# Kernel tuning notes

Measured on AMD Instinct MI355X. Metric: run time of the kernel, lower is better.

The kernel has to match this reference:

```python
import jax, jax.numpy as jnp
import numpy as np

N, E = 50000, 800000
IN, H, OUT = 128, 128, 64
N_MID = 4  # middle GIN layers (num_layers=6 -> 1 first + 4 mid + 1 last)


def setup_inputs() -> dict:
    key = jax.random.key(0)
    ks = jax.random.split(key, 8)
    def w(k, shape, fan_in):
        return (jax.random.normal(k, shape, jnp.float32) / np.sqrt(fan_in)).astype(jnp.float32)
    x = jax.random.normal(ks[0], (N, IN), jnp.float32)
    edge_index = jax.random.randint(ks[1], (2, E), 0, N, dtype=jnp.int64)
    return {
        "x": x,
        "edge_index": edge_index,
        "w0a": w(ks[2], (IN, H), IN), "b0a": jnp.zeros((H,), jnp.float32),
        "w0b": w(ks[3], (H, H), H),   "b0b": jnp.zeros((H,), jnp.float32),
        "wma": w(ks[4], (N_MID, H, H), H), "bma": jnp.zeros((N_MID, H), jnp.float32),
        "wmb": w(ks[5], (N_MID, H, H), H), "bmb": jnp.zeros((N_MID, H), jnp.float32),
        "wl": w(ks[6], (H, OUT), H), "bl": jnp.zeros((OUT,), jnp.float32),
    }


def reference(x, edge_index, w0a, b0a, w0b, b0b, wma, bma, wmb, bmb, wl, bl):
    n = x.shape[0]
    src, dst = edge_index[0], edge_index[1]

    def gin_agg(h):
        # GIN with eps=0: (1+eps)*h_i + sum_{j->i} h_j
        return h + jax.ops.segment_sum(h[src], dst, num_segments=n)

    # layer 0: Lin(IN,H)-ReLU-Lin(H,H), then inter-layer ReLU
    h = gin_agg(x)
    h = jax.nn.relu(jax.nn.relu(h @ w0a + b0a) @ w0b + b0b)

    # middle layers 1..4 (scan over stacked params)
    def body(h, p):
        wa, ba, wb, bb = p
        g = gin_agg(h)
        g = jax.nn.relu(g @ wa + ba) @ wb + bb
        return jax.nn.relu(g), None

    h, _ = jax.lax.scan(body, h, (wma, bma, wmb, bmb))

    # last layer: single Lin(H,OUT), then sigmoid
    h = gin_agg(h) @ wl + bl
    return jax.nn.sigmoid(h)
```

## Files before the change

kernel.cpp:

```cpp
#include <hip/hip_runtime.h>
#include <hip/hip_bf16.h>

#define HDIM 128

typedef __attribute__((ext_vector_type(8))) short bf16x8;
typedef __attribute__((ext_vector_type(4))) float f32x4;

__device__ __forceinline__ unsigned short bf16_rne(float x) {
    unsigned int u = __float_as_uint(x);
    unsigned int r = u + 0x7FFFu + ((u >> 16) & 1u);
    return (unsigned short)(r >> 16);
}


__global__ __launch_bounds__(256) void hist_kernel(const int* __restrict__ ei, int E,
                                                   int* __restrict__ deg) {
    int e = blockIdx.x * 256 + threadIdx.x;
    if (e < E) atomicAdd(&deg[ei[E + e]], 1);
}

__global__ __launch_bounds__(256) void scan1_kernel(const int* __restrict__ deg,
                                                    int* __restrict__ rowp,
                                                    int* __restrict__ bsum, int N) {
    __shared__ int s[256];
    int t = threadIdx.x;
    int i = blockIdx.x * 256 + t;
    int v = (i < N) ? deg[i] : 0;
    s[t] = v; __syncthreads();
    for (int off = 1; off < 256; off <<= 1) {
        int x = (t >= off) ? s[t - off] : 0;
        __syncthreads();
        s[t] += x;
        __syncthreads();
    }
    if (i < N) rowp[i] = s[t] - v;
    if (t == 255) bsum[blockIdx.x] = s[255];
}

__global__ __launch_bounds__(256) void scan2_kernel(int* __restrict__ bsum, int NB) {
    __shared__ int s[256];
    int t = threadIdx.x;
    int v = (t < NB) ? bsum[t] : 0;
    s[t] = v; __syncthreads();
    for (int off = 1; off < 256; off <<= 1) {
        int x = (t >= off) ? s[t - off] : 0;
        __syncthreads();
        s[t] += x;
        __syncthreads();
    }
    if (t < NB) bsum[t] = s[t] - v;
}

__global__ __launch_bounds__(256) void scan3_kernel(int* __restrict__ rowp,
                                                    const int* __restrict__ bsum,
                                                    int* __restrict__ cur, int N, int E) {
    int i = blockIdx.x * 256 + threadIdx.x;
    if (i < N) {
        int r = rowp[i] + bsum[blockIdx.x];
        rowp[i] = r;
        cur[i] = r;
    }
    if (i == 0) rowp[N] = E;
}

template <typename IT>
__global__ __launch_bounds__(256) void scatter_kernel(const int* __restrict__ ei, int E,
                                                      int* __restrict__ cur,
                                                      IT* __restrict__ srcs) {
    int e = blockIdx.x * 256 + threadIdx.x;
    if (e < E) {
        int d = ei[E + e];
        int p = atomicAdd(&cur[d], 1);
        srcs[p] = (IT)ei[e];
    }
}


__global__ __launch_bounds__(256) void pack_w_kernel(const float* __restrict__ w0a,
                                                     const float* __restrict__ w0b,
                                                     const float* __restrict__ wma,
                                                     const float* __restrict__ wmb,
                                                     short* __restrict__ wpack) {
    int idx = blockIdx.x * 256 + threadIdx.x;
    if (idx >= 10 * 16384) return;
    int mat = idx >> 14;
    int rem = idx & 16383;
    int i = rem & 7;
    int lane = (rem >> 3) & 63;
    int kc = (rem >> 9) & 3;
    int ct = rem >> 11;
    const float* W = (mat == 0) ? w0a
                   : (mat == 1) ? w0b
                   : (mat < 6)  ? (wma + (size_t)(mat - 2) * 16384)
                                : (wmb + (size_t)(mat - 6) * 16384);
    int k = kc * 32 + (lane >> 4) * 8 + i;
    int col = ct * 16 + (lane & 15);
    float x = W[k * 128 + col];
    unsigned short hb = bf16_rne(x);
    float hf = __uint_as_float(((unsigned int)hb) << 16);
    unsigned short lb = bf16_rne(x - hf);
    wpack[(size_t)mat * 32768 + rem] = (short)hb;
    wpack[(size_t)mat * 32768 + 16384 + rem] = (short)lb;
}


template <typename IT>
__global__ __launch_bounds__(256) void agg_slice_kernel(const float* __restrict__ h,
                                                        const int* __restrict__ rowp,
                                                        const IT* __restrict__ srcs,
                                                        float* __restrict__ out, int N) {
    const int tid = threadIdx.x;
    const int g = blockIdx.x & 7;
    const int chunk = blockIdx.x >> 3;
    const int grp = tid >> 2;
    const int l = tid & 3;
    const int node = chunk * 64 + grp;
    if (node >= N) return;

    const float4* h4 = (const float4*)h;
    const int cbase = g * 4 + l;

    int beg = rowp[node], end = rowp[node + 1];
    int em1 = max(end - 1, 0);

    const float4 z = {0.f, 0.f, 0.f, 0.f};
    float4 a0 = h4[(size_t)node * 32 + cbase];
    float4 a1 = z, a2 = z, a3 = z, a4 = z, a5 = z, a6 = z, a7 = z;

    for (int q = beg; q < end; q += 8) {
        int c0 = min(q + 0, em1);
        int c1 = min(q + 1, em1);
        int c2 = min(q + 2, em1);
        int c3 = min(q + 3, em1);
        int c4 = min(q + 4, em1);
        int c5 = min(q + 5, em1);
        int c6 = min(q + 6, em1);
        int c7 = min(q + 7, em1);
        int s0 = (int)srcs[c0];
        int s1 = (int)srcs[c1];
        int s2 = (int)srcs[c2];
        int s3 = (int)srcs[c3];
        int s4 = (int)srcs[c4];
        int s5 = (int)srcs[c5];
        int s6 = (int)srcs[c6];
        int s7 = (int)srcs[c7];
        float4 v0 = h4[(size_t)s0 * 32 + cbase];
        float4 v1 = h4[(size_t)s1 * 32 + cbase];
        float4 v2 = h4[(size_t)s2 * 32 + cbase];
        float4 v3 = h4[(size_t)s3 * 32 + cbase];
        float4 v4 = h4[(size_t)s4 * 32 + cbase];
        float4 v5 = h4[(size_t)s5 * 32 + cbase];
        float4 v6 = h4[(size_t)s6 * 32 + cbase];
        float4 v7 = h4[(size_t)s7 * 32 + cbase];
        float m0 = (q + 0 < end) ? 1.f : 0.f;
        float m1 = (q + 1 < end) ? 1.f : 0.f;
        float m2 = (q + 2 < end) ? 1.f : 0.f;
        float m3 = (q + 3 < end) ? 1.f : 0.f;
        float m4 = (q + 4 < end) ? 1.f : 0.f;
        float m5 = (q + 5 < end) ? 1.f : 0.f;
        float m6 = (q + 6 < end) ? 1.f : 0.f;
        float m7 = (q + 7 < end) ? 1.f : 0.f;
        a0.x = fmaf(v0.x, m0, a0.x); a0.y = fmaf(v0.y, m0, a0.y);
        a0.z = fmaf(v0.z, m0, a0.z); a0.w = fmaf(v0.w, m0, a0.w);
        a1.x = fmaf(v1.x, m1, a1.x); a1.y = fmaf(v1.y, m1, a1.y);
        a1.z = fmaf(v1.z, m1, a1.z); a1.w = fmaf(v1.w, m1, a1.w);
        a2.x = fmaf(v2.x, m2, a2.x); a2.y = fmaf(v2.y, m2, a2.y);
        a2.z = fmaf(v2.z, m2, a2.z); a2.w = fmaf(v2.w, m2, a2.w);
        a3.x = fmaf(v3.x, m3, a3.x); a3.y = fmaf(v3.y, m3, a3.y);
        a3.z = fmaf(v3.z, m3, a3.z); a3.w = fmaf(v3.w, m3, a3.w);
        a4.x = fmaf(v4.x, m4, a4.x); a4.y = fmaf(v4.y, m4, a4.y);
        a4.z = fmaf(v4.z, m4, a4.z); a4.w = fmaf(v4.w, m4, a4.w);
        a5.x = fmaf(v5.x, m5, a5.x); a5.y = fmaf(v5.y, m5, a5.y);
        a5.z = fmaf(v5.z, m5, a5.z); a5.w = fmaf(v5.w, m5, a5.w);
        a6.x = fmaf(v6.x, m6, a6.x); a6.y = fmaf(v6.y, m6, a6.y);
        a6.z = fmaf(v6.z, m6, a6.z); a6.w = fmaf(v6.w, m6, a6.w);
        a7.x = fmaf(v7.x, m7, a7.x); a7.y = fmaf(v7.y, m7, a7.y);
        a7.z = fmaf(v7.z, m7, a7.z); a7.w = fmaf(v7.w, m7, a7.w);
    }

    a0.x = ((a0.x + a1.x) + (a2.x + a3.x)) + ((a4.x + a5.x) + (a6.x + a7.x));
    a0.y = ((a0.y + a1.y) + (a2.y + a3.y)) + ((a4.y + a5.y) + (a6.y + a7.y));
    a0.z = ((a0.z + a1.z) + (a2.z + a3.z)) + ((a4.z + a5.z) + (a6.z + a7.z));
    a0.w = ((a0.w + a1.w) + (a2.w + a3.w)) + ((a4.w + a5.w) + (a6.w + a7.w));
    ((float4*)out)[(size_t)node * 32 + cbase] = a0;
}


template <typename IT>
__global__ __launch_bounds__(256) void agg_out_kernel(const float* __restrict__ t,
                                                      const int* __restrict__ rowp,
                                                      const IT* __restrict__ srcs,
                                                      const float* __restrict__ bias,
                                                      float* __restrict__ out, int N) {
    int lane = threadIdx.x & 63;
    int node = blockIdx.x * 4 + (threadIdx.x >> 6);
    if (node >= N) return;
    int beg = rowp[node], end = rowp[node + 1];
    float a0 = t[node * 64 + lane];
    float a1 = 0.f, a2 = 0.f, a3 = 0.f, a4 = 0.f, a5 = 0.f, a6 = 0.f, a7 = 0.f;
    int p = beg;
    for (; p + 8 <= end; p += 8) {
        int s0 = (int)srcs[p + 0];
        int s1 = (int)srcs[p + 1];
        int s2 = (int)srcs[p + 2];
        int s3 = (int)srcs[p + 3];
        int s4 = (int)srcs[p + 4];
        int s5 = (int)srcs[p + 5];
        int s6 = (int)srcs[p + 6];
        int s7 = (int)srcs[p + 7];
        a0 += t[s0 * 64 + lane];
        a1 += t[s1 * 64 + lane];
        a2 += t[s2 * 64 + lane];
        a3 += t[s3 * 64 + lane];
        a4 += t[s4 * 64 + lane];
        a5 += t[s5 * 64 + lane];
        a6 += t[s6 * 64 + lane];
        a7 += t[s7 * 64 + lane];
    }
    for (; p < end; ++p) a0 += t[(int)srcs[p] * 64 + lane];
    float z = a0 + ((a1 + a2) + (a3 + a4)) + ((a5 + a6) + a7) + bias[lane];
    out[node * 64 + lane] = 1.f / (1.f + __expf(-z));
}


__device__ __forceinline__ void cvt8(const float4 p, const float4 q,
                                     bf16x8& hi, bf16x8& lo) {
    unsigned short hb; float hf;
#define CVT1(IDX, V) \
    hb = bf16_rne(V); hf = __uint_as_float(((unsigned int)hb) << 16); \
    hi[IDX] = (short)hb; lo[IDX] = (short)bf16_rne((V) - hf);
    CVT1(0, p.x) CVT1(1, p.y) CVT1(2, p.z) CVT1(3, p.w)
    CVT1(4, q.x) CVT1(5, q.y) CVT1(6, q.z) CVT1(7, q.w)
#undef CVT1
}

template <bool WRITE_GLOBAL>
__device__ __forceinline__ void gemm_phase_mfma(float* __restrict__ myrows,
                                                const short* __restrict__ wp,
                                                const float* __restrict__ bias,
                                                int arow, int agrp,
                                                int l, float* __restrict__ gout,
                                                int row_base, int N) {
    f32x4 acc[8];
#pragma unroll
    for (int ct = 0; ct < 8; ++ct) acc[ct] = (f32x4){0.f, 0.f, 0.f, 0.f};

    const short* wlo = wp + 16384;
#pragma unroll
    for (int kc = 0; kc < 4; ++kc) {
        const float* ap = &myrows[arow * 132 + kc * 32 + agrp * 8];
        float4 p = *(const float4*)ap;
        float4 q = *(const float4*)(ap + 4);
        bf16x8 ahi, alo;
        cvt8(p, q, ahi, alo);
#pragma unroll
        for (int ct = 0; ct < 8; ++ct) {
            const int off = ((ct * 4 + kc) << 9) + (l << 3);
            bf16x8 bhi = *(const bf16x8*)(wp + off);
            bf16x8 blo = *(const bf16x8*)(wlo + off);
            acc[ct] = __builtin_amdgcn_mfma_f32_16x16x32_bf16(ahi, bhi, acc[ct], 0, 0, 0);
            acc[ct] = __builtin_amdgcn_mfma_f32_16x16x32_bf16(alo, bhi, acc[ct], 0, 0, 0);
            acc[ct] = __builtin_amdgcn_mfma_f32_16x16x32_bf16(ahi, blo, acc[ct], 0, 0, 0);
            acc[ct] = __builtin_amdgcn_mfma_f32_16x16x32_bf16(alo, blo, acc[ct], 0, 0, 0);
        }
    }

#pragma unroll
    for (int ct = 0; ct < 8; ++ct) {
        float bv = bias[ct * 16 + arow];
#pragma unroll
        for (int r = 0; r < 4; ++r) {
            float v = fmaxf(acc[ct][r] + bv, 0.f);
            if (WRITE_GLOBAL) {
                int row = row_base + agrp * 4 + r;
                if (row < N) gout[(size_t)row * 128 + ct * 16 + arow] = v;
            } else {
                myrows[(agrp * 4 + r) * 132 + ct * 16 + arow] = v;
            }
        }
    }
}

__global__ __launch_bounds__(256, 4) void mlp2_mfma_kernel(
    const float* __restrict__ in,
    const short* __restrict__ wpa, const float* __restrict__ ba,
    const short* __restrict__ wpb, const float* __restrict__ bb,
    float* __restrict__ out, int N) {
    __shared__ float sh[64 * 132];
    const int tid = threadIdx.x;
    const int wave = tid >> 6;
    const int l = tid & 63;
    const int arow = l & 15;
    const int agrp = l >> 4;
    const int row0 = blockIdx.x * 64;

    const float4* in4 = (const float4*)in;
#pragma unroll
    for (int it = 0; it < 8; ++it) {
        int i = tid + it * 256;
        int r = i >> 5, c = i & 31;
        int row = row0 + r;
        float4 z = {0.f, 0.f, 0.f, 0.f};
        float4 v = (row < N) ? in4[(size_t)row * 32 + c] : z;
        *(float4*)&sh[r * 132 + c * 4] = v;
    }
    __syncthreads();

    float* myrows = &sh[wave * 16 * 132];
    gemm_phase_mfma<false>(myrows, wpa, ba, arow, agrp, l, nullptr, 0, N);
    __syncthreads();
    gemm_phase_mfma<true>(myrows, wpb, bb, arow, agrp, l, out, row0 + wave * 16, N);
}


__global__ __launch_bounds__(256, 6) void gemm64_kernel(const float* __restrict__ in,
                                                        const float* __restrict__ W,
                                                        float* __restrict__ out, int N) {
    constexpr int TX = 16, RPT = 2;
    __shared__ float4 sh[32 * 32];

    int tid = threadIdx.x;
    int tx = tid % TX;
    int ty = tid / TX;
    int row0 = blockIdx.x * 32;

    const float4* in4 = (const float4*)in;
    for (int i = tid; i < 32 * 32; i += 256) {
        int r = i >> 5, c = i & 31;
        int row = row0 + r;
        float4 z = {0.f, 0.f, 0.f, 0.f};
        sh[i] = (row < N) ? in4[(size_t)row * 32 + c] : z;
    }
    __syncthreads();

    const float4* W4 = (const float4*)W;
    float acc[RPT][4];
#pragma unroll
    for (int r = 0; r < RPT; ++r)
#pragma unroll
        for (int c = 0; c < 4; ++c) acc[r][c] = 0.f;

#pragma unroll 4
    for (int kk = 0; kk < 128; kk += 4) {
        float4 w0 = W4[(kk + 0) * TX + tx];
        float4 w1 = W4[(kk + 1) * TX + tx];
        float4 w2 = W4[(kk + 2) * TX + tx];
        float4 w3 = W4[(kk + 3) * TX + tx];
#pragma unroll
        for (int r = 0; r < RPT; ++r) {
            float4 hv = sh[(ty * RPT + r) * 32 + (kk >> 2)];
            acc[r][0] += hv.x * w0.x + hv.y * w1.x + hv.z * w2.x + hv.w * w3.x;
            acc[r][1] += hv.x * w0.y + hv.y * w1.y + hv.z * w2.y + hv.w * w3.y;
            acc[r][2] += hv.x * w0.z + hv.y * w1.z + hv.z * w2.z + hv.w * w3.z;
            acc[r][3] += hv.x * w0.w + hv.y * w1.w + hv.z * w2.w + hv.w * w3.w;
        }
    }

#pragma unroll
    for (int r = 0; r < RPT; ++r) {
        int row = row0 + ty * RPT + r;
        if (row < N) {
            float4 v = {acc[r][0], acc[r][1], acc[r][2], acc[r][3]};
            ((float4*)out)[(size_t)row * TX + tx] = v;
        }
    }
}


template <typename IT>
static void run_graph(const float* x, const int* ei, int N, int E,
                      const float* w0a, const float* b0a, const float* w0b, const float* b0b,
                      const float* wma, const float* bma, const float* wmb, const float* bmb,
                      const float* wl, const float* bl,
                      float* A, float* B, int* deg, int* rowp, int* cur, int* bsum,
                      IT* srcs, short* wpack, float* out, hipStream_t stream) {
    const int NB = (N + 255) / 256;
    dim3 blk(256);

    pack_w_kernel<<<(10 * 16384 + 255) / 256, blk, 0, stream>>>(w0a, w0b, wma, wmb, wpack);

    hipMemsetAsync(deg, 0, (size_t)N * sizeof(int), stream);
    hist_kernel<<<(E + 255) / 256, blk, 0, stream>>>(ei, E, deg);
    scan1_kernel<<<NB, blk, 0, stream>>>(deg, rowp, bsum, N);
    scan2_kernel<<<1, blk, 0, stream>>>(bsum, NB);
    scan3_kernel<<<NB, blk, 0, stream>>>(rowp, bsum, cur, N, E);
    scatter_kernel<IT><<<(E + 255) / 256, blk, 0, stream>>>(ei, E, cur, srcs);

    const int slice_grid = 8 * ((N + 63) / 64);
    const int aggo_grid  = (N + 3) / 4;
    const int m64_grid   = (N + 63) / 64;
    const int g32_grid   = (N + 31) / 32;

    agg_slice_kernel<IT><<<slice_grid, blk, 0, stream>>>(x, rowp, srcs, A, N);
    mlp2_mfma_kernel<<<m64_grid, blk, 0, stream>>>(A, wpack + 0, b0a,
                                                   wpack + 32768, b0b, B, N);

    float* h = B;
    float* o = A;
    for (int l = 0; l < 4; ++l) {
        const short* wpa = wpack + (size_t)(2 + l) * 32768;
        const short* wpb = wpack + (size_t)(6 + l) * 32768;
        const float* ba = bma + (size_t)l * HDIM;
        const float* bb = bmb + (size_t)l * HDIM;
        agg_slice_kernel<IT><<<slice_grid, blk, 0, stream>>>(h, rowp, srcs, o, N);
        mlp2_mfma_kernel<<<m64_grid, blk, 0, stream>>>(o, wpa, ba, wpb, bb, h, N);
    }

    gemm64_kernel<<<g32_grid, blk, 0, stream>>>(h, wl, o, N);
    agg_out_kernel<IT><<<aggo_grid, blk, 0, stream>>>(o, rowp, srcs, bl, out, N);
}

extern "C" void kernel_launch(void* const* d_in, const int* in_sizes, int n_in,
                              void* d_out, int out_size, void* d_ws, size_t ws_size,
                              hipStream_t stream) {
    const float* x   = (const float*)d_in[0];
    const int*   ei  = (const int*)d_in[1];
    const float* w0a = (const float*)d_in[2];
    const float* b0a = (const float*)d_in[3];
    const float* w0b = (const float*)d_in[4];
    const float* b0b = (const float*)d_in[5];
    const float* wma = (const float*)d_in[6];
    const float* bma = (const float*)d_in[7];
    const float* wmb = (const float*)d_in[8];
    const float* bmb = (const float*)d_in[9];
    const float* wl  = (const float*)d_in[10];
    const float* bl  = (const float*)d_in[11];

    const int N = in_sizes[0] / HDIM;
    const int E = in_sizes[1] / 2;

    float* A = (float*)d_ws;
    float* B = A + (size_t)N * HDIM;
    int* deg  = (int*)(B + (size_t)N * HDIM);
    int* rowp = deg + N;
    int* cur  = rowp + N + 1;
    int* bsum = cur + N;
    int* srcs = bsum + 256;
    short* wpack = (short*)(srcs + E);

    if (N <= 65535) {
        run_graph<unsigned short>(x, ei, N, E, w0a, b0a, w0b, b0b, wma, bma, wmb, bmb,
                                  wl, bl, A, B, deg, rowp, cur, bsum,
                                  (unsigned short*)srcs, wpack, (float*)d_out, stream);
    } else {
        run_graph<int>(x, ei, N, E, w0a, b0a, w0b, b0b, wma, bma, wmb, bmb,
                       wl, bl, A, B, deg, rowp, cur, bsum,
                       srcs, wpack, (float*)d_out, stream);
    }
}
```

Before: 666.5 us.

## Make aggregation persistent with XCD-affine feature-slice work queues

Replaces the fixed-grid feature-slice aggregation with a persistent kernel of 2048 blocks. Each block reads its hardware XCC id and first drains an atomic work queue for the matching 16-column feature slice, then moves on to the other slices. The aim is to keep each slice's gathered rows in a single XCD's L2 cache and to balance work dynamically. In exchange it adds a global atomic and two block barriers per 64-node chunk, plus per-layer counters that must be zeroed with a memset.

```diff
diff --git a/kernel.cpp b/kernel.cpp
--- a/kernel.cpp
+++ b/kernel.cpp
@@ -105,84 +105,97 @@
 
 
 template <typename IT>
-__global__ __launch_bounds__(256) void agg_slice_kernel(const float* __restrict__ h,
-                                                        const int* __restrict__ rowp,
-                                                        const IT* __restrict__ srcs,
-                                                        float* __restrict__ out, int N) {
+__global__ __launch_bounds__(256) void agg_xcd_kernel(const float* __restrict__ h,
+                                                      const int* __restrict__ rowp,
+                                                      const IT* __restrict__ srcs,
+                                                      float* __restrict__ out, int N,
+                                                      int* __restrict__ cnt) {
+    __shared__ int s_task;
+    const int nchunks = (N + 63) >> 6;
     const int tid = threadIdx.x;
-    const int g = blockIdx.x & 7;
-    const int chunk = blockIdx.x >> 3;
     const int grp = tid >> 2;
     const int l = tid & 3;
-    const int node = chunk * 64 + grp;
-    if (node >= N) return;
+
+    int myx = __builtin_amdgcn_s_getreg(20 | (0 << 6) | (31 << 11)) & 7;
 
     const float4* h4 = (const float4*)h;
-    const int cbase = g * 4 + l;
-
-    int beg = rowp[node], end = rowp[node + 1];
-    int em1 = max(end - 1, 0);
-
-    const float4 z = {0.f, 0.f, 0.f, 0.f};
-    float4 a0 = h4[(size_t)node * 32 + cbase];
-    float4 a1 = z, a2 = z, a3 = z, a4 = z, a5 = z, a6 = z, a7 = z;
-
-    for (int q = beg; q < end; q += 8) {
-        int c0 = min(q + 0, em1);
-        int c1 = min(q + 1, em1);
-        int c2 = min(q + 2, em1);
-        int c3 = min(q + 3, em1);
-        int c4 = min(q + 4, em1);
-        int c5 = min(q + 5, em1);
-        int c6 = min(q + 6, em1);
-        int c7 = min(q + 7, em1);
-        int s0 = (int)srcs[c0];
-        int s1 = (int)srcs[c1];
-        int s2 = (int)srcs[c2];
-        int s3 = (int)srcs[c3];
-        int s4 = (int)srcs[c4];
-        int s5 = (int)srcs[c5];
-        int s6 = (int)srcs[c6];
-        int s7 = (int)srcs[c7];
-        float4 v0 = h4[(size_t)s0 * 32 + cbase];
-        float4 v1 = h4[(size_t)s1 * 32 + cbase];
-        float4 v2 = h4[(size_t)s2 * 32 + cbase];
-        float4 v3 = h4[(size_t)s3 * 32 + cbase];
-        float4 v4 = h4[(size_t)s4 * 32 + cbase];
-        float4 v5 = h4[(size_t)s5 * 32 + cbase];
-        float4 v6 = h4[(size_t)s6 * 32 + cbase];
-        float4 v7 = h4[(size_t)s7 * 32 + cbase];
-        float m0 = (q + 0 < end) ? 1.f : 0.f;
-        float m1 = (q + 1 < end) ? 1.f : 0.f;
-        float m2 = (q + 2 < end) ? 1.f : 0.f;
-        float m3 = (q + 3 < end) ? 1.f : 0.f;
-        float m4 = (q + 4 < end) ? 1.f : 0.f;
-        float m5 = (q + 5 < end) ? 1.f : 0.f;
-        float m6 = (q + 6 < end) ? 1.f : 0.f;
-        float m7 = (q + 7 < end) ? 1.f : 0.f;
-        a0.x = fmaf(v0.x, m0, a0.x); a0.y = fmaf(v0.y, m0, a0.y);
-        a0.z = fmaf(v0.z, m0, a0.z); a0.w = fmaf(v0.w, m0, a0.w);
-        a1.x = fmaf(v1.x, m1, a1.x); a1.y = fmaf(v1.y, m1, a1.y);
-        a1.z = fmaf(v1.z, m1, a1.z); a1.w = fmaf(v1.w, m1, a1.w);
-        a2.x = fmaf(v2.x, m2, a2.x); a2.y = fmaf(v2.y, m2, a2.y);
-        a2.z = fmaf(v2.z, m2, a2.z); a2.w = fmaf(v2.w, m2, a2.w);
-        a3.x = fmaf(v3.x, m3, a3.x); a3.y = fmaf(v3.y, m3, a3.y);
-        a3.z = fmaf(v3.z, m3, a3.z); a3.w = fmaf(v3.w, m3, a3.w);
-        a4.x = fmaf(v4.x, m4, a4.x); a4.y = fmaf(v4.y, m4, a4.y);
-        a4.z = fmaf(v4.z, m4, a4.z); a4.w = fmaf(v4.w, m4, a4.w);
-        a5.x = fmaf(v5.x, m5, a5.x); a5.y = fmaf(v5.y, m5, a5.y);
-        a5.z = fmaf(v5.z, m5, a5.z); a5.w = fmaf(v5.w, m5, a5.w);
-        a6.x = fmaf(v6.x, m6, a6.x); a6.y = fmaf(v6.y, m6, a6.y);
-        a6.z = fmaf(v6.z, m6, a6.z); a6.w = fmaf(v6.w, m6, a6.w);
-        a7.x = fmaf(v7.x, m7, a7.x); a7.y = fmaf(v7.y, m7, a7.y);
-        a7.z = fmaf(v7.z, m7, a7.z); a7.w = fmaf(v7.w, m7, a7.w);
-    }
-
-    a0.x = ((a0.x + a1.x) + (a2.x + a3.x)) + ((a4.x + a5.x) + (a6.x + a7.x));
-    a0.y = ((a0.y + a1.y) + (a2.y + a3.y)) + ((a4.y + a5.y) + (a6.y + a7.y));
-    a0.z = ((a0.z + a1.z) + (a2.z + a3.z)) + ((a4.z + a5.z) + (a6.z + a7.z));
-    a0.w = ((a0.w + a1.w) + (a2.w + a3.w)) + ((a4.w + a5.w) + (a6.w + a7.w));
-    ((float4*)out)[(size_t)node * 32 + cbase] = a0;
+
+    for (int gi = 0; gi < 8; ++gi) {
+        const int g = (myx + gi) & 7;
+        const int cbase = g * 4 + l;
+        for (;;) {
+            if (tid == 0) s_task = atomicAdd(&cnt[g], 1);
+            __syncthreads();
+            const int t = s_task;
+            __syncthreads();
+            if (t >= nchunks) break;
+
+            const int node = t * 64 + grp;
+            if (node < N) {
+                int beg = rowp[node], end = rowp[node + 1];
+                int em1 = max(end - 1, 0);
+                const float4 z = {0.f, 0.f, 0.f, 0.f};
+                float4 a0 = h4[(size_t)node * 32 + cbase];
+                float4 a1 = z, a2 = z, a3 = z, a4 = z, a5 = z, a6 = z, a7 = z;
+
+                for (int q = beg; q < end; q += 8) {
+                    int c0 = min(q + 0, em1);
+                    int c1 = min(q + 1, em1);
+                    int c2 = min(q + 2, em1);
+                    int c3 = min(q + 3, em1);
+                    int c4 = min(q + 4, em1);
+                    int c5 = min(q + 5, em1);
+                    int c6 = min(q + 6, em1);
+                    int c7 = min(q + 7, em1);
+                    int s0 = (int)srcs[c0];
+                    int s1 = (int)srcs[c1];
+                    int s2 = (int)srcs[c2];
+                    int s3 = (int)srcs[c3];
+                    int s4 = (int)srcs[c4];
+                    int s5 = (int)srcs[c5];
+                    int s6 = (int)srcs[c6];
+                    int s7 = (int)srcs[c7];
+                    float4 v0 = h4[(size_t)s0 * 32 + cbase];
+                    float4 v1 = h4[(size_t)s1 * 32 + cbase];
+                    float4 v2 = h4[(size_t)s2 * 32 + cbase];
+                    float4 v3 = h4[(size_t)s3 * 32 + cbase];
+                    float4 v4 = h4[(size_t)s4 * 32 + cbase];
+                    float4 v5 = h4[(size_t)s5 * 32 + cbase];
+                    float4 v6 = h4[(size_t)s6 * 32 + cbase];
+                    float4 v7 = h4[(size_t)s7 * 32 + cbase];
+                    float m0 = (q + 0 < end) ? 1.f : 0.f;
+                    float m1 = (q + 1 < end) ? 1.f : 0.f;
+                    float m2 = (q + 2 < end) ? 1.f : 0.f;
+                    float m3 = (q + 3 < end) ? 1.f : 0.f;
+                    float m4 = (q + 4 < end) ? 1.f : 0.f;
+                    float m5 = (q + 5 < end) ? 1.f : 0.f;
+                    float m6 = (q + 6 < end) ? 1.f : 0.f;
+                    float m7 = (q + 7 < end) ? 1.f : 0.f;
+                    a0.x = fmaf(v0.x, m0, a0.x); a0.y = fmaf(v0.y, m0, a0.y);
+                    a0.z = fmaf(v0.z, m0, a0.z); a0.w = fmaf(v0.w, m0, a0.w);
+                    a1.x = fmaf(v1.x, m1, a1.x); a1.y = fmaf(v1.y, m1, a1.y);
+                    a1.z = fmaf(v1.z, m1, a1.z); a1.w = fmaf(v1.w, m1, a1.w);
+                    a2.x = fmaf(v2.x, m2, a2.x); a2.y = fmaf(v2.y, m2, a2.y);
+                    a2.z = fmaf(v2.z, m2, a2.z); a2.w = fmaf(v2.w, m2, a2.w);
+                    a3.x = fmaf(v3.x, m3, a3.x); a3.y = fmaf(v3.y, m3, a3.y);
+                    a3.z = fmaf(v3.z, m3, a3.z); a3.w = fmaf(v3.w, m3, a3.w);
+                    a4.x = fmaf(v4.x, m4, a4.x); a4.y = fmaf(v4.y, m4, a4.y);
+                    a4.z = fmaf(v4.z, m4, a4.z); a4.w = fmaf(v4.w, m4, a4.w);
+                    a5.x = fmaf(v5.x, m5, a5.x); a5.y = fmaf(v5.y, m5, a5.y);
+                    a5.z = fmaf(v5.z, m5, a5.z); a5.w = fmaf(v5.w, m5, a5.w);
+                    a6.x = fmaf(v6.x, m6, a6.x); a6.y = fmaf(v6.y, m6, a6.y);
+                    a6.z = fmaf(v6.z, m6, a6.z); a6.w = fmaf(v6.w, m6, a6.w);
+                    a7.x = fmaf(v7.x, m7, a7.x); a7.y = fmaf(v7.y, m7, a7.y);
+                    a7.z = fmaf(v7.z, m7, a7.z); a7.w = fmaf(v7.w, m7, a7.w);
+                }
+                a0.x = ((a0.x + a1.x) + (a2.x + a3.x)) + ((a4.x + a5.x) + (a6.x + a7.x));
+                a0.y = ((a0.y + a1.y) + (a2.y + a3.y)) + ((a4.y + a5.y) + (a6.y + a7.y));
+                a0.z = ((a0.z + a1.z) + (a2.z + a3.z)) + ((a4.z + a5.z) + (a6.z + a7.z));
+                a0.w = ((a0.w + a1.w) + (a2.w + a3.w)) + ((a4.w + a5.w) + (a6.w + a7.w));
+                ((float4*)out)[(size_t)node * 32 + cbase] = a0;
+            }
+        }
+    }
 }
 
 
@@ -373,25 +386,26 @@
                       const float* wma, const float* bma, const float* wmb, const float* bmb,
                       const float* wl, const float* bl,
                       float* A, float* B, int* deg, int* rowp, int* cur, int* bsum,
-                      IT* srcs, short* wpack, float* out, hipStream_t stream) {
+                      IT* srcs, short* wpack, int* qcnt, float* out, hipStream_t stream) {
     const int NB = (N + 255) / 256;
     dim3 blk(256);
 
     pack_w_kernel<<<(10 * 16384 + 255) / 256, blk, 0, stream>>>(w0a, w0b, wma, wmb, wpack);
 
     hipMemsetAsync(deg, 0, (size_t)N * sizeof(int), stream);
+    hipMemsetAsync(qcnt, 0, 5 * 8 * sizeof(int), stream);
     hist_kernel<<<(E + 255) / 256, blk, 0, stream>>>(ei, E, deg);
     scan1_kernel<<<NB, blk, 0, stream>>>(deg, rowp, bsum, N);
     scan2_kernel<<<1, blk, 0, stream>>>(bsum, NB);
     scan3_kernel<<<NB, blk, 0, stream>>>(rowp, bsum, cur, N, E);
     scatter_kernel<IT><<<(E + 255) / 256, blk, 0, stream>>>(ei, E, cur, srcs);
 
-    const int slice_grid = 8 * ((N + 63) / 64);
-    const int aggo_grid  = (N + 3) / 4;
-    const int m64_grid   = (N + 63) / 64;
-    const int g32_grid   = (N + 31) / 32;
-
-    agg_slice_kernel<IT><<<slice_grid, blk, 0, stream>>>(x, rowp, srcs, A, N);
+    const int agg_grid  = 2048;
+    const int aggo_grid = (N + 3) / 4;
+    const int m64_grid  = (N + 63) / 64;
+    const int g32_grid  = (N + 31) / 32;
+
+    agg_xcd_kernel<IT><<<agg_grid, blk, 0, stream>>>(x, rowp, srcs, A, N, qcnt + 0);
     mlp2_mfma_kernel<<<m64_grid, blk, 0, stream>>>(A, wpack + 0, b0a,
                                                    wpack + 32768, b0b, B, N);
 
@@ -402,7 +416,8 @@
         const short* wpb = wpack + (size_t)(6 + l) * 32768;
         const float* ba = bma + (size_t)l * HDIM;
         const float* bb = bmb + (size_t)l * HDIM;
-        agg_slice_kernel<IT><<<slice_grid, blk, 0, stream>>>(h, rowp, srcs, o, N);
+        agg_xcd_kernel<IT><<<agg_grid, blk, 0, stream>>>(h, rowp, srcs, o, N,
+                                                         qcnt + 8 * (l + 1));
         mlp2_mfma_kernel<<<m64_grid, blk, 0, stream>>>(o, wpa, ba, wpb, bb, h, N);
     }
 
@@ -437,14 +452,16 @@
     int* bsum = cur + N;
     int* srcs = bsum + 256;
     short* wpack = (short*)(srcs + E);
+    int* qcnt = (int*)(wpack + 10 * 32768);
 
     if (N <= 65535) {
         run_graph<unsigned short>(x, ei, N, E, w0a, b0a, w0b, b0b, wma, bma, wmb, bmb,
                                   wl, bl, A, B, deg, rowp, cur, bsum,
-                                  (unsigned short*)srcs, wpack, (float*)d_out, stream);
+                                  (unsigned short*)srcs, wpack, qcnt,
+                                  (float*)d_out, stream);
     } else {
         run_graph<int>(x, ei, N, E, w0a, b0a, w0b, b0b, wma, bma, wmb, bmb,
                        wl, bl, A, B, deg, rowp, cur, bsum,
-                       srcs, wpack, (float*)d_out, stream);
-    }
-}
+                       srcs, wpack, qcnt, (float*)d_out, stream);
+    }
+}
```

New measurement: 1.704 ms. 156% more time.
